# Kernel tuning notes

Hardware: AMD Instinct MI355X
Metric: run time of the kernel (lower is better)

## Reference

```python
import jax, jax.numpy as jnp
import numpy as np

B, L, K = 8, 1024, 30
NUM_RBF = 16
NPOS = 16
MAXREL = 32
EDGE = 128
EDGE_IN = NPOS + NUM_RBF * 25  # 416

# 25 atom-pair order (ProteinMPNN convention) over atoms [Ca=0, N=1, C=2, O=3, Cb=4]
PAIR_I = np.array([0,1,2,3,4,0,0,0,0,1,1,1,4,4,3,1,2,3,4,2,3,4,2,3,2])
PAIR_J = np.array([0,1,2,3,4,1,2,3,4,2,3,4,2,3,2,0,0,0,0,1,1,1,4,4,3])


def setup_inputs() -> dict:
    key = jax.random.key(0)
    ks = jax.random.split(key, 8)
    X = jax.random.normal(ks[0], (B, L, 4, 3), dtype=jnp.float32) * 3.0
    mask = jnp.ones((B, L), dtype=jnp.float32)
    residue_idx = jnp.arange(B * L, dtype=jnp.int64 if jax.config.jax_enable_x64 else jnp.int32).reshape(B, L)
    S = jax.random.randint(ks[1], (B, L), 0, 21)
    SSE3_seq = jax.random.randint(ks[2], (B, L), 0, 4)
    SSE8_seq = jax.random.randint(ks[3], (B, L), 0, 9)
    W_pos = jax.random.normal(ks[4], (2 * MAXREL + 2, NPOS), dtype=jnp.float32) * 0.02
    b_pos = jnp.zeros((NPOS,), dtype=jnp.float32)
    W_edge = jax.random.normal(ks[5], (EDGE_IN, EDGE), dtype=jnp.float32) * 0.02
    ln_gamma = jnp.ones((EDGE,), dtype=jnp.float32)
    ln_beta = jnp.zeros((EDGE,), dtype=jnp.float32)
    return {"X": X, "mask": mask, "residue_idx": residue_idx, "S": S,
            "SSE3_seq": SSE3_seq, "SSE8_seq": SSE8_seq,
            "W_pos": W_pos, "b_pos": b_pos, "W_edge": W_edge,
            "ln_gamma": ln_gamma, "ln_beta": ln_beta}


def _forward(X, mask, residue_idx, W_pos, b_pos, W_edge, ln_gamma, ln_beta):
    N = X[:, :, 0, :]
    Ca = X[:, :, 1, :]
    C = X[:, :, 2, :]
    O = X[:, :, 3, :]
    b = Ca - N
    c = C - Ca
    a = jnp.cross(b, c)
    Cb = -0.58273431 * a + 0.56802827 * b - 0.54067466 * c + Ca

    # _dist: masked pairwise Ca distances, k smallest
    mask2 = mask[:, :, None] * mask[:, None, :]                      # [B,L,L]
    D = mask2 * jnp.sqrt(jnp.sum((Ca[:, :, None] - Ca[:, None]) ** 2, -1) + 1e-6)
    D_max = jnp.max(D, axis=-1, keepdims=True)
    D_adjust = D + (1.0 - mask2) * D_max
    _, E_idx = jax.lax.top_k(-D_adjust, K)                           # [B,L,K] smallest

    # 25 atom-pair RBFs: gather neighbor atoms, then pairwise atom distances
    atoms = jnp.stack([Ca, N, C, O, Cb], axis=2)                     # [B,L,5,3]
    atoms_nb = jax.vmap(lambda a, i: a[i])(atoms, E_idx)             # [B,L,K,5,3]
    Dp = jnp.sqrt(jnp.sum((atoms[:, :, None, :, None, :] - atoms_nb[:, :, :, None, :, :]) ** 2, -1) + 1e-6)  # [B,L,K,5,5]
    mu = jnp.linspace(2.0, 22.0, NUM_RBF)
    sigma = (22.0 - 2.0) / NUM_RBF
    rbf = jnp.exp(-(((Dp[..., None] - mu) / sigma) ** 2))            # [B,L,K,5,5,R]
    rbf_all = rbf[:, :, :, PAIR_I, PAIR_J, :].reshape(Dp.shape[0], Dp.shape[1], K, 25 * NUM_RBF)

    # positional encodings of relative residue index
    offset = residue_idx[:, :, None] - residue_idx[:, None, :]       # [B,L,L]
    off_nb = jnp.take_along_axis(offset, E_idx, axis=2)              # [B,L,K]
    d = jnp.clip(off_nb + MAXREL, 0, 2 * MAXREL)
    E_pos = W_pos[d] + b_pos                                         # [B,L,K,NPOS]

    E = jnp.concatenate([E_pos, rbf_all], axis=-1) @ W_edge          # [B,L,K,EDGE]
    m = jnp.mean(E, axis=-1, keepdims=True)
    v = jnp.mean((E - m) ** 2, axis=-1, keepdims=True)
    E = (E - m) / jnp.sqrt(v + 1e-5) * ln_gamma + ln_beta
    return E, E_idx


def reference(X, mask, residue_idx, S, SSE3_seq, SSE8_seq, W_pos, b_pos, W_edge, ln_gamma, ln_beta):
    return _forward(X, mask, residue_idx, W_pos, b_pos, W_edge, ln_gamma, ln_beta)
```

## Files before the change

### kernel.cpp

```cpp
#include <hip/hip_runtime.h>

#define BB 8
#define LL 1024
#define KNB 30
#define NUM_RBF 16
#define NPOS 16
#define MAXREL 32
#define EDGE_C 128
#define EDGE_IN 416
#define NKK 26
#define WTF_N (NKK * 4 * 64 * 8)

__constant__ int PAIR_I_d[25] = {0,1,2,3,4,0,0,0,0,1,1,1,4,4,3,1,2,3,4,2,3,4,2,3,2};
__constant__ int PAIR_J_d[25] = {0,1,2,3,4,1,2,3,4,2,3,4,2,3,2,0,0,0,0,1,1,1,4,4,3};

typedef float floatx16 __attribute__((ext_vector_type(16)));

__global__ __launch_bounds__(256) void knn_kernel(const float* __restrict__ X,
                                                  const float* __restrict__ mask,
                                                  float* __restrict__ out_idx,
                                                  const float* __restrict__ W_edge,
                                                  unsigned char* __restrict__ WtF) {
    if (blockIdx.x >= 2048) {
        int o = (blockIdx.x - 2048) * 256 + threadIdx.x;
        if (o < WTF_N) {
            int j = o & 7, l = (o >> 3) & 63, w = (o >> 9) & 3, kk = o >> 11;
            int k = (kk << 4) + ((l >> 5) << 3) + j;
            int n = (w << 5) + (l & 31);
            float wv = W_edge[k * EDGE_C + n];
            int pk = __builtin_amdgcn_cvt_pk_fp8_f32(wv, wv, 0, false);
            WtF[o] = (unsigned char)(pk & 0xFF);
        }
        return;
    }

    int b = blockIdx.x >> 8;
    int i0 = (blockIdx.x & 255) * 4;
    int tid = threadIdx.x;
    int lane = tid & 63;
    int wv = tid >> 6;

    __shared__ float sCa[LL * 3];
    __shared__ float sMask[LL];

    for (int j = tid; j < LL; j += 256) {
        int base = (b * LL + j) * 12 + 3;
        sCa[j * 3 + 0] = X[base + 0];
        sCa[j * 3 + 1] = X[base + 1];
        sCa[j * 3 + 2] = X[base + 2];
        sMask[j] = mask[b * LL + j];
    }
    __syncthreads();

    int i = i0 + wv;
    int row = b * LL + i;
    float cax = sCa[i * 3 + 0], cay = sCa[i * 3 + 1], caz = sCa[i * 3 + 2];
    float mi = sMask[i];

    float Dv[16];
    float dmax = 0.0f;
#pragma unroll
    for (int c = 0; c < 16; ++c) {
        int j = lane + c * 64;
        float dx = cax - sCa[j * 3 + 0];
        float dy = cay - sCa[j * 3 + 1];
        float dz = caz - sCa[j * 3 + 2];
        float m2 = mi * sMask[j];
        float D = m2 * sqrtf(dx * dx + dy * dy + dz * dz + 1e-6f);
        Dv[c] = D;
        dmax = fmaxf(dmax, D);
    }
    for (int o = 32; o; o >>= 1) dmax = fmaxf(dmax, __shfl_down(dmax, o));
    dmax = __shfl(dmax, 0);

    double cand[16];
#pragma unroll
    for (int c = 0; c < 16; ++c) {
        int j = lane + c * 64;
        float m2 = mi * sMask[j];
        float Dadj = Dv[c] + (1.0f - m2) * dmax;
        unsigned int bits = __float_as_uint(Dadj);
        cand[c] = fma((double)bits, 1024.0, (double)j);
    }

    const double KILL = 9.0e15;
    float myj = 0.0f;
    for (int r = 0; r < KNB; ++r) {
        double a0 = fmin(cand[0], cand[1]);
        double a1 = fmin(cand[2], cand[3]);
        double a2 = fmin(cand[4], cand[5]);
        double a3 = fmin(cand[6], cand[7]);
        double a4 = fmin(cand[8], cand[9]);
        double a5 = fmin(cand[10], cand[11]);
        double a6 = fmin(cand[12], cand[13]);
        double a7 = fmin(cand[14], cand[15]);
        a0 = fmin(a0, a1); a2 = fmin(a2, a3); a4 = fmin(a4, a5); a6 = fmin(a6, a7);
        a0 = fmin(a0, a2); a4 = fmin(a4, a6);
        double m = fmin(a0, a4);
        for (int o = 32; o; o >>= 1) {
            double other = __shfl_down(m, o);
            m = fmin(m, other);
        }
        m = __shfl(m, 0);
        unsigned long long ku = (unsigned long long)m;
        int jw = __builtin_amdgcn_readfirstlane((int)(ku & 1023));
        bool own = (lane == (jw & 63));
        switch (jw >> 6) {
            case 0:  if (own) cand[0]  = KILL; break;
            case 1:  if (own) cand[1]  = KILL; break;
            case 2:  if (own) cand[2]  = KILL; break;
            case 3:  if (own) cand[3]  = KILL; break;
            case 4:  if (own) cand[4]  = KILL; break;
            case 5:  if (own) cand[5]  = KILL; break;
            case 6:  if (own) cand[6]  = KILL; break;
            case 7:  if (own) cand[7]  = KILL; break;
            case 8:  if (own) cand[8]  = KILL; break;
            case 9:  if (own) cand[9]  = KILL; break;
            case 10: if (own) cand[10] = KILL; break;
            case 11: if (own) cand[11] = KILL; break;
            case 12: if (own) cand[12] = KILL; break;
            case 13: if (own) cand[13] = KILL; break;
            case 14: if (own) cand[14] = KILL; break;
            case 15: if (own) cand[15] = KILL; break;
        }
        if (lane == r) myj = (float)jw;
    }
    if (lane < KNB) out_idx[(size_t)row * KNB + lane] = myj;
}

__global__ __launch_bounds__(256) void edge_kernel(const float* __restrict__ X,
                                                   const int* __restrict__ ridx,
                                                   const float* __restrict__ W_pos,
                                                   const float* __restrict__ b_pos,
                                                   const unsigned char* __restrict__ WtF,
                                                   const float* __restrict__ gamma,
                                                   const float* __restrict__ beta,
                                                   const float* __restrict__ out_idx,
                                                   float* __restrict__ out_E) {
    int row = blockIdx.x;
    int b = row >> 10;
    int i = row & 1023;
    int tid = threadIdx.x;

    __shared__ __align__(16) char smem[16384];
    unsigned char* fA = (unsigned char*)smem;
    float* Esh = (float*)smem;
    float* atoms = (float*)smem;
    float* dist = (float*)(smem + 13312);

    if (tid < 31) {
        int r = (tid == 0) ? i : (int)out_idx[(size_t)row * KNB + (tid - 1)];
        int base = (b * LL + r) * 12;
        float Nx = X[base + 0], Ny = X[base + 1], Nz = X[base + 2];
        float Cax = X[base + 3], Cay = X[base + 4], Caz = X[base + 5];
        float Cx = X[base + 6], Cy = X[base + 7], Cz = X[base + 8];
        float Ox = X[base + 9], Oy = X[base + 10], Oz = X[base + 11];
        float bx = Cax - Nx, by = Cay - Ny, bz = Caz - Nz;
        float cx = Cx - Cax, cy = Cy - Cay, cz = Cz - Caz;
        float ax = by * cz - bz * cy;
        float ay = bz * cx - bx * cz;
        float az = bx * cy - by * cx;
        float Cbx = -0.58273431f * ax + 0.56802827f * bx - 0.54067466f * cx + Cax;
        float Cby = -0.58273431f * ay + 0.56802827f * by - 0.54067466f * cy + Cay;
        float Cbz = -0.58273431f * az + 0.56802827f * bz - 0.54067466f * cz + Caz;
        float* A = &atoms[tid * 15];
        A[0] = Cax; A[1] = Cay; A[2] = Caz;
        A[3] = Nx;  A[4] = Ny;  A[5] = Nz;
        A[6] = Cx;  A[7] = Cy;  A[8] = Cz;
        A[9] = Ox;  A[10] = Oy; A[11] = Oz;
        A[12] = Cbx; A[13] = Cby; A[14] = Cbz;
    }
    __syncthreads();

    for (int idx = tid; idx < KNB * 25; idx += 256) {
        int k = idx / 25;
        int p = idx - k * 25;
        const float* Ai = &atoms[PAIR_I_d[p] * 3];
        const float* Aj = &atoms[(1 + k) * 15 + PAIR_J_d[p] * 3];
        float dx = Ai[0] - Aj[0], dy = Ai[1] - Aj[1], dz = Ai[2] - Aj[2];
        dist[idx] = __builtin_amdgcn_sqrtf(dx * dx + dy * dy + dz * dz + 1e-6f);
    }
    __syncthreads();

    {
        int m = tid & 31;
        int kgb = tid >> 5;
        float cbase = (kgb & 1) ? 14.4f : 5.8666668f;
        const float SQL2E = 1.2011224f;
        const float C1 = 3.0777494f;
        const float C0 = 1.6414664f;
        const float DK = 0.1027397f;
#pragma unroll
        for (int r = 0; r < 7; ++r) {
            int kg = kgb + 8 * r;
            if (kg < 52) {
                int lo, hi;
                if (m >= KNB) {
                    lo = 0; hi = 0;
                } else if (kg < 2) {
                    int jn = (int)out_idx[(size_t)row * KNB + m];
                    int off = ridx[row] - ridx[b * LL + jn] + MAXREL;
                    off = off < 0 ? 0 : (off > 2 * MAXREL ? 2 * MAXREL : off);
                    const float4* wp = (const float4*)&W_pos[off * NPOS + kg * 8];
                    const float4* bp = (const float4*)&b_pos[kg * 8];
                    float4 w0 = wp[0], w1 = wp[1];
                    float4 p0 = bp[0], p1 = bp[1];
                    lo = __builtin_amdgcn_cvt_pk_fp8_f32(w0.x + p0.x, w0.y + p0.y, 0, false);
                    lo = __builtin_amdgcn_cvt_pk_fp8_f32(w0.z + p0.z, w0.w + p0.w, lo, true);
                    hi = __builtin_amdgcn_cvt_pk_fp8_f32(w1.x + p1.x, w1.y + p1.y, 0, false);
                    hi = __builtin_amdgcn_cvt_pk_fp8_f32(w1.z + p1.z, w1.w + p1.w, hi, true);
                } else {
                    int p = (kg - 2) >> 1;
                    float d = dist[m * 25 + p];
                    float xc = fminf(fmaf(0.8f, d, -cbase), 12.0f);
                    float xs = xc * SQL2E;
                    float r4 = __builtin_amdgcn_exp2f(-xs * xs);
                    float fw = __builtin_amdgcn_exp2f(fmaf(C1, xc, -C0));
                    float bw = __builtin_amdgcn_exp2f(fmaf(-C1, xc, -C0));
                    float r5 = r4 * fw; fw *= DK;
                    float r6 = r5 * fw; fw *= DK;
                    float r7 = r6 * fw;
                    float r3 = r4 * bw; bw *= DK;
                    float r2 = r3 * bw; bw *= DK;
                    float r1 = r2 * bw; bw *= DK;
                    float r0 = r1 * bw;
                    lo = __builtin_amdgcn_cvt_pk_fp8_f32(r0, r1, 0, false);
                    lo = __builtin_amdgcn_cvt_pk_fp8_f32(r2, r3, lo, true);
                    hi = __builtin_amdgcn_cvt_pk_fp8_f32(r4, r5, 0, false);
                    hi = __builtin_amdgcn_cvt_pk_fp8_f32(r6, r7, hi, true);
                }
                int pos = ((kg >> 1) * 64 + m + 32 * (kg & 1)) * 8;
                long v = ((long)(unsigned int)hi << 32) | (unsigned int)lo;
                *(long*)(fA + pos) = v;
            }
        }
    }
    __syncthreads();

    int wv = tid >> 6;
    int l = tid & 63;
    floatx16 acc;
#pragma unroll
    for (int r = 0; r < 16; ++r) acc[r] = 0.0f;

    const long* Ap = (const long*)fA + l;
    const long* Bp = (const long*)WtF + wv * 64 + l;
#pragma unroll 4
    for (int kk = 0; kk < NKK; ++kk) {
        long a = Ap[kk * 64];
        long bfr = Bp[kk * 256];
        acc = __builtin_amdgcn_mfma_f32_32x32x16_fp8_fp8(a, bfr, acc, 0, 0, 0);
    }
    __syncthreads();

#pragma unroll
    for (int r = 0; r < 16; ++r) {
        int rr = (r & 3) + 8 * (r >> 2) + 4 * (l >> 5);
        Esh[rr * EDGE_C + wv * 32 + (l & 31)] = acc[r];
    }
    __syncthreads();

    int cg = tid & 31;
    int ky = tid >> 5;
    int c0 = cg * 4;
    float gam0 = gamma[c0 + 0], gam1 = gamma[c0 + 1];
    float gam2 = gamma[c0 + 2], gam3 = gamma[c0 + 3];
    float bet0 = beta[c0 + 0], bet1 = beta[c0 + 1];
    float bet2 = beta[c0 + 2], bet3 = beta[c0 + 3];

#pragma unroll
    for (int r2 = 0; r2 < 4; ++r2) {
        int e = ky + 8 * r2;
        float4 v = *(const float4*)&Esh[e * EDGE_C + c0];
        float s = (v.x + v.y) + (v.z + v.w);
        float q = fmaf(v.x, v.x, fmaf(v.y, v.y, fmaf(v.z, v.z, v.w * v.w)));
#pragma unroll
        for (int o = 16; o; o >>= 1) {
            s += __shfl_xor(s, o);
            q += __shfl_xor(q, o);
        }
        float mean = s * 0.0078125f;
        float var = fmaf(-mean, mean, q * 0.0078125f);
        float inv = __builtin_amdgcn_rsqf(var + 1e-5f);
        if (e < KNB) {
            float ig0 = inv * gam0, ig1 = inv * gam1;
            float ig2 = inv * gam2, ig3 = inv * gam3;
            float4 o4;
            o4.x = fmaf(v.x, ig0, fmaf(-mean, ig0, bet0));
            o4.y = fmaf(v.y, ig1, fmaf(-mean, ig1, bet1));
            o4.z = fmaf(v.z, ig2, fmaf(-mean, ig2, bet2));
            o4.w = fmaf(v.w, ig3, fmaf(-mean, ig3, bet3));
            *(float4*)(out_E + ((size_t)(row * KNB + e)) * EDGE_C + c0) = o4;
        }
    }
}

extern "C" void kernel_launch(void* const* d_in, const int* in_sizes, int n_in,
                              void* d_out, int out_size, void* d_ws, size_t ws_size,
                              hipStream_t stream) {
    const float* X      = (const float*)d_in[0];
    const float* mask   = (const float*)d_in[1];
    const int*   ridx   = (const int*)d_in[2];
    const float* W_pos  = (const float*)d_in[6];
    const float* b_pos  = (const float*)d_in[7];
    const float* W_edge = (const float*)d_in[8];
    const float* gamma  = (const float*)d_in[9];
    const float* beta   = (const float*)d_in[10];

    float* out_E   = (float*)d_out;
    float* out_idx = out_E + (size_t)BB * LL * KNB * EDGE_C;
    unsigned char* WtF = (unsigned char*)d_ws;

    int knn_grid = 2048 + (WTF_N + 255) / 256;
    knn_kernel<<<knn_grid, 256, 0, stream>>>(X, mask, out_idx, W_edge, WtF);
    edge_kernel<<<BB * LL, 256, 0, stream>>>(X, ridx, W_pos, b_pos, WtF,
                                             gamma, beta, out_idx, out_E);
}
```

Measured before the change: 238.5 us.

## Fuse kNN selection and edge feature kernels into one per-4-row kernel

Merges the kNN top-k kernel and the edge RBF/MFMA/layernorm kernel into a single kernel in which each 256-thread block finds neighbors for 4 residues and then processes those 4 rows sequentially. Neighbor indices are passed through shared memory instead of a global round trip, and the weight fp8 prep moves into a separate small kernel. This removes one large launch and the reload of neighbor indices, but cuts the edge-stage grid to a quarter of its previous block count, with four serialized passes per block and more barriers, so occupancy and latency hiding may drop.

Result: slower. 267.7 us (+12.2%).

```diff
diff --git a/kernel.cpp b/kernel.cpp
--- a/kernel.cpp
+++ b/kernel.cpp
@@ -16,32 +16,44 @@
 
 typedef float floatx16 __attribute__((ext_vector_type(16)));
 
-__global__ __launch_bounds__(256) void knn_kernel(const float* __restrict__ X,
-                                                  const float* __restrict__ mask,
-                                                  float* __restrict__ out_idx,
-                                                  const float* __restrict__ W_edge,
-                                                  unsigned char* __restrict__ WtF) {
-    if (blockIdx.x >= 2048) {
-        int o = (blockIdx.x - 2048) * 256 + threadIdx.x;
-        if (o < WTF_N) {
-            int j = o & 7, l = (o >> 3) & 63, w = (o >> 9) & 3, kk = o >> 11;
-            int k = (kk << 4) + ((l >> 5) << 3) + j;
-            int n = (w << 5) + (l & 31);
-            float wv = W_edge[k * EDGE_C + n];
-            int pk = __builtin_amdgcn_cvt_pk_fp8_f32(wv, wv, 0, false);
-            WtF[o] = (unsigned char)(pk & 0xFF);
-        }
-        return;
+__global__ __launch_bounds__(256) void wprep_kernel(const float* __restrict__ W_edge,
+                                                    unsigned char* __restrict__ WtF) {
+    int o = blockIdx.x * 256 + threadIdx.x;
+    if (o < WTF_N) {
+        int j = o & 7, l = (o >> 3) & 63, w = (o >> 9) & 3, kk = o >> 11;
+        int k = (kk << 4) + ((l >> 5) << 3) + j;
+        int n = (w << 5) + (l & 31);
+        float wv = W_edge[k * EDGE_C + n];
+        int pk = __builtin_amdgcn_cvt_pk_fp8_f32(wv, wv, 0, false);
+        WtF[o] = (unsigned char)(pk & 0xFF);
     }
-
+}
+
+__global__ __launch_bounds__(256) void fused_kernel(const float* __restrict__ X,
+                                                    const float* __restrict__ mask,
+                                                    const int* __restrict__ ridx,
+                                                    const float* __restrict__ W_pos,
+                                                    const float* __restrict__ b_pos,
+                                                    const unsigned char* __restrict__ WtF,
+                                                    const float* __restrict__ gamma,
+                                                    const float* __restrict__ beta,
+                                                    float* __restrict__ out_idx,
+                                                    float* __restrict__ out_E) {
     int b = blockIdx.x >> 8;
     int i0 = (blockIdx.x & 255) * 4;
     int tid = threadIdx.x;
     int lane = tid & 63;
     int wv = tid >> 6;
-
-    __shared__ float sCa[LL * 3];
-    __shared__ float sMask[LL];
+    int l = lane;
+
+    __shared__ __align__(16) char smem[16896];
+    float* sCa  = (float*)smem;
+    float* sMask = (float*)(smem + 12288);
+    int*   nbrL = (int*)(smem + 16384);
+    unsigned char* fA = (unsigned char*)smem;
+    float* Esh = (float*)smem;
+    float* atoms = (float*)smem;
+    float* dist = (float*)(smem + 13312);
 
     for (int j = tid; j < LL; j += 256) {
         int base = (b * LL + j) * 12 + 3;
@@ -52,214 +64,88 @@
     }
     __syncthreads();
 
-    int i = i0 + wv;
-    int row = b * LL + i;
-    float cax = sCa[i * 3 + 0], cay = sCa[i * 3 + 1], caz = sCa[i * 3 + 2];
-    float mi = sMask[i];
-
-    float Dv[16];
-    float dmax = 0.0f;
-#pragma unroll
-    for (int c = 0; c < 16; ++c) {
-        int j = lane + c * 64;
-        float dx = cax - sCa[j * 3 + 0];
-        float dy = cay - sCa[j * 3 + 1];
-        float dz = caz - sCa[j * 3 + 2];
-        float m2 = mi * sMask[j];
-        float D = m2 * sqrtf(dx * dx + dy * dy + dz * dz + 1e-6f);
-        Dv[c] = D;
-        dmax = fmaxf(dmax, D);
-    }
-    for (int o = 32; o; o >>= 1) dmax = fmaxf(dmax, __shfl_down(dmax, o));
-    dmax = __shfl(dmax, 0);
-
-    double cand[16];
-#pragma unroll
-    for (int c = 0; c < 16; ++c) {
-        int j = lane + c * 64;
-        float m2 = mi * sMask[j];
-        float Dadj = Dv[c] + (1.0f - m2) * dmax;
-        unsigned int bits = __float_as_uint(Dadj);
-        cand[c] = fma((double)bits, 1024.0, (double)j);
-    }
-
-    const double KILL = 9.0e15;
-    float myj = 0.0f;
-    for (int r = 0; r < KNB; ++r) {
-        double a0 = fmin(cand[0], cand[1]);
-        double a1 = fmin(cand[2], cand[3]);
-        double a2 = fmin(cand[4], cand[5]);
-        double a3 = fmin(cand[6], cand[7]);
-        double a4 = fmin(cand[8], cand[9]);
-        double a5 = fmin(cand[10], cand[11]);
-        double a6 = fmin(cand[12], cand[13]);
-        double a7 = fmin(cand[14], cand[15]);
-        a0 = fmin(a0, a1); a2 = fmin(a2, a3); a4 = fmin(a4, a5); a6 = fmin(a6, a7);
-        a0 = fmin(a0, a2); a4 = fmin(a4, a6);
-        double m = fmin(a0, a4);
-        for (int o = 32; o; o >>= 1) {
-            double other = __shfl_down(m, o);
-            m = fmin(m, other);
-        }
-        m = __shfl(m, 0);
-        unsigned long long ku = (unsigned long long)m;
-        int jw = __builtin_amdgcn_readfirstlane((int)(ku & 1023));
-        bool own = (lane == (jw & 63));
-        switch (jw >> 6) {
-            case 0:  if (own) cand[0]  = KILL; break;
-            case 1:  if (own) cand[1]  = KILL; break;
-            case 2:  if (own) cand[2]  = KILL; break;
-            case 3:  if (own) cand[3]  = KILL; break;
-            case 4:  if (own) cand[4]  = KILL; break;
-            case 5:  if (own) cand[5]  = KILL; break;
-            case 6:  if (own) cand[6]  = KILL; break;
-            case 7:  if (own) cand[7]  = KILL; break;
-            case 8:  if (own) cand[8]  = KILL; break;
-            case 9:  if (own) cand[9]  = KILL; break;
-            case 10: if (own) cand[10] = KILL; break;
-            case 11: if (own) cand[11] = KILL; break;
-            case 12: if (own) cand[12] = KILL; break;
-            case 13: if (own) cand[13] = KILL; break;
-            case 14: if (own) cand[14] = KILL; break;
-            case 15: if (own) cand[15] = KILL; break;
-        }
-        if (lane == r) myj = (float)jw;
-    }
-    if (lane < KNB) out_idx[(size_t)row * KNB + lane] = myj;
-}
-
-__global__ __launch_bounds__(256) void edge_kernel(const float* __restrict__ X,
-                                                   const int* __restrict__ ridx,
-                                                   const float* __restrict__ W_pos,
-                                                   const float* __restrict__ b_pos,
-                                                   const unsigned char* __restrict__ WtF,
-                                                   const float* __restrict__ gamma,
-                                                   const float* __restrict__ beta,
-                                                   const float* __restrict__ out_idx,
-                                                   float* __restrict__ out_E) {
-    int row = blockIdx.x;
-    int b = row >> 10;
-    int i = row & 1023;
-    int tid = threadIdx.x;
-
-    __shared__ __align__(16) char smem[16384];
-    unsigned char* fA = (unsigned char*)smem;
-    float* Esh = (float*)smem;
-    float* atoms = (float*)smem;
-    float* dist = (float*)(smem + 13312);
-
-    if (tid < 31) {
-        int r = (tid == 0) ? i : (int)out_idx[(size_t)row * KNB + (tid - 1)];
-        int base = (b * LL + r) * 12;
-        float Nx = X[base + 0], Ny = X[base + 1], Nz = X[base + 2];
-        float Cax = X[base + 3], Cay = X[base + 4], Caz = X[base + 5];
-        float Cx = X[base + 6], Cy = X[base + 7], Cz = X[base + 8];
-        float Ox = X[base + 9], Oy = X[base + 10], Oz = X[base + 11];
-        float bx = Cax - Nx, by = Cay - Ny, bz = Caz - Nz;
-        float cx = Cx - Cax, cy = Cy - Cay, cz = Cz - Caz;
-        float ax = by * cz - bz * cy;
-        float ay = bz * cx - bx * cz;
-        float az = bx * cy - by * cx;
-        float Cbx = -0.58273431f * ax + 0.56802827f * bx - 0.54067466f * cx + Cax;
-        float Cby = -0.58273431f * ay + 0.56802827f * by - 0.54067466f * cy + Cay;
-        float Cbz = -0.58273431f * az + 0.56802827f * bz - 0.54067466f * cz + Caz;
-        float* A = &atoms[tid * 15];
-        A[0] = Cax; A[1] = Cay; A[2] = Caz;
-        A[3] = Nx;  A[4] = Ny;  A[5] = Nz;
-        A[6] = Cx;  A[7] = Cy;  A[8] = Cz;
-        A[9] = Ox;  A[10] = Oy; A[11] = Oz;
-        A[12] = Cbx; A[13] = Cby; A[14] = Cbz;
+    {
+        int i = i0 + wv;
+        int row = b * LL + i;
+        float cax = sCa[i * 3 + 0], cay = sCa[i * 3 + 1], caz = sCa[i * 3 + 2];
+        float mi = sMask[i];
+
+        float Dv[16];
+        float dmax = 0.0f;
+#pragma unroll
+        for (int c = 0; c < 16; ++c) {
+            int j = lane + c * 64;
+            float dx = cax - sCa[j * 3 + 0];
+            float dy = cay - sCa[j * 3 + 1];
+            float dz = caz - sCa[j * 3 + 2];
+            float m2 = mi * sMask[j];
+            float D = m2 * sqrtf(dx * dx + dy * dy + dz * dz + 1e-6f);
+            Dv[c] = D;
+            dmax = fmaxf(dmax, D);
+        }
+        for (int o = 32; o; o >>= 1) dmax = fmaxf(dmax, __shfl_down(dmax, o));
+        dmax = __shfl(dmax, 0);
+
+        double cand[16];
+#pragma unroll
+        for (int c = 0; c < 16; ++c) {
+            int j = lane + c * 64;
+            float m2 = mi * sMask[j];
+            float Dadj = Dv[c] + (1.0f - m2) * dmax;
+            unsigned int bits = __float_as_uint(Dadj);
+            cand[c] = fma((double)bits, 1024.0, (double)j);
+        }
+
+        const double KILL = 9.0e15;
+        float myj = 0.0f;
+        for (int r = 0; r < KNB; ++r) {
+            double a0 = fmin(cand[0], cand[1]);
+            double a1 = fmin(cand[2], cand[3]);
+            double a2 = fmin(cand[4], cand[5]);
+            double a3 = fmin(cand[6], cand[7]);
+            double a4 = fmin(cand[8], cand[9]);
+            double a5 = fmin(cand[10], cand[11]);
+            double a6 = fmin(cand[12], cand[13]);
+            double a7 = fmin(cand[14], cand[15]);
+            a0 = fmin(a0, a1); a2 = fmin(a2, a3); a4 = fmin(a4, a5); a6 = fmin(a6, a7);
+            a0 = fmin(a0, a2); a4 = fmin(a4, a6);
+            double m = fmin(a0, a4);
+            for (int o = 32; o; o >>= 1) {
+                double other = __shfl_down(m, o);
+                m = fmin(m, other);
+            }
+            m = __shfl(m, 0);
+            unsigned long long ku = (unsigned long long)m;
+            int jw = __builtin_amdgcn_readfirstlane((int)(ku & 1023));
+            bool own = (lane == (jw & 63));
+            switch (jw >> 6) {
+                case 0:  if (own) cand[0]  = KILL; break;
+                case 1:  if (own) cand[1]  = KILL; break;
+                case 2:  if (own) cand[2]  = KILL; break;
+                case 3:  if (own) cand[3]  = KILL; break;
+                case 4:  if (own) cand[4]  = KILL; break;
+                case 5:  if (own) cand[5]  = KILL; break;
+                case 6:  if (own) cand[6]  = KILL; break;
+                case 7:  if (own) cand[7]  = KILL; break;
+                case 8:  if (own) cand[8]  = KILL; break;
+                case 9:  if (own) cand[9]  = KILL; break;
+                case 10: if (own) cand[10] = KILL; break;
+                case 11: if (own) cand[11] = KILL; break;
+                case 12: if (own) cand[12] = KILL; break;
+                case 13: if (own) cand[13] = KILL; break;
+                case 14: if (own) cand[14] = KILL; break;
+                case 15: if (own) cand[15] = KILL; break;
+            }
+            if (lane == r) myj = (float)jw;
+        }
+        if (lane < KNB) {
+            out_idx[(size_t)row * KNB + lane] = myj;
+            nbrL[wv * KNB + lane] = (int)myj;
+        }
     }
     __syncthreads();
 
-    for (int idx = tid; idx < KNB * 25; idx += 256) {
-        int k = idx / 25;
-        int p = idx - k * 25;
-        const float* Ai = &atoms[PAIR_I_d[p] * 3];
-        const float* Aj = &atoms[(1 + k) * 15 + PAIR_J_d[p] * 3];
-        float dx = Ai[0] - Aj[0], dy = Ai[1] - Aj[1], dz = Ai[2] - Aj[2];
-        dist[idx] = __builtin_amdgcn_sqrtf(dx * dx + dy * dy + dz * dz + 1e-6f);
-    }
-    __syncthreads();
-
-    {
-        int m = tid & 31;
-        int kgb = tid >> 5;
-        float cbase = (kgb & 1) ? 14.4f : 5.8666668f;
-        const float SQL2E = 1.2011224f;
-        const float C1 = 3.0777494f;
-        const float C0 = 1.6414664f;
-        const float DK = 0.1027397f;
-#pragma unroll
-        for (int r = 0; r < 7; ++r) {
-            int kg = kgb + 8 * r;
-            if (kg < 52) {
-                int lo, hi;
-                if (m >= KNB) {
-                    lo = 0; hi = 0;
-                } else if (kg < 2) {
-                    int jn = (int)out_idx[(size_t)row * KNB + m];
-                    int off = ridx[row] - ridx[b * LL + jn] + MAXREL;
-                    off = off < 0 ? 0 : (off > 2 * MAXREL ? 2 * MAXREL : off);
-                    const float4* wp = (const float4*)&W_pos[off * NPOS + kg * 8];
-                    const float4* bp = (const float4*)&b_pos[kg * 8];
-                    float4 w0 = wp[0], w1 = wp[1];
-                    float4 p0 = bp[0], p1 = bp[1];
-                    lo = __builtin_amdgcn_cvt_pk_fp8_f32(w0.x + p0.x, w0.y + p0.y, 0, false);
-                    lo = __builtin_amdgcn_cvt_pk_fp8_f32(w0.z + p0.z, w0.w + p0.w, lo, true);
-                    hi = __builtin_amdgcn_cvt_pk_fp8_f32(w1.x + p1.x, w1.y + p1.y, 0, false);
-                    hi = __builtin_amdgcn_cvt_pk_fp8_f32(w1.z + p1.z, w1.w + p1.w, hi, true);
-                } else {
-                    int p = (kg - 2) >> 1;
-                    float d = dist[m * 25 + p];
-                    float xc = fminf(fmaf(0.8f, d, -cbase), 12.0f);
-                    float xs = xc * SQL2E;
-                    float r4 = __builtin_amdgcn_exp2f(-xs * xs);
-                    float fw = __builtin_amdgcn_exp2f(fmaf(C1, xc, -C0));
-                    float bw = __builtin_amdgcn_exp2f(fmaf(-C1, xc, -C0));
-                    float r5 = r4 * fw; fw *= DK;
-                    float r6 = r5 * fw; fw *= DK;
-                    float r7 = r6 * fw;
-                    float r3 = r4 * bw; bw *= DK;
-                    float r2 = r3 * bw; bw *= DK;
-                    float r1 = r2 * bw; bw *= DK;
-                    float r0 = r1 * bw;
-                    lo = __builtin_amdgcn_cvt_pk_fp8_f32(r0, r1, 0, false);
-                    lo = __builtin_amdgcn_cvt_pk_fp8_f32(r2, r3, lo, true);
-                    hi = __builtin_amdgcn_cvt_pk_fp8_f32(r4, r5, 0, false);
-                    hi = __builtin_amdgcn_cvt_pk_fp8_f32(r6, r7, hi, true);
-                }
-                int pos = ((kg >> 1) * 64 + m + 32 * (kg & 1)) * 8;
-                long v = ((long)(unsigned int)hi << 32) | (unsigned int)lo;
-                *(long*)(fA + pos) = v;
-            }
-        }
-    }
-    __syncthreads();
-
-    int wv = tid >> 6;
-    int l = tid & 63;
-    floatx16 acc;
-#pragma unroll
-    for (int r = 0; r < 16; ++r) acc[r] = 0.0f;
-
-    const long* Ap = (const long*)fA + l;
     const long* Bp = (const long*)WtF + wv * 64 + l;
-#pragma unroll 4
-    for (int kk = 0; kk < NKK; ++kk) {
-        long a = Ap[kk * 64];
-        long bfr = Bp[kk * 256];
-        acc = __builtin_amdgcn_mfma_f32_32x32x16_fp8_fp8(a, bfr, acc, 0, 0, 0);
-    }
-    __syncthreads();
-
-#pragma unroll
-    for (int r = 0; r < 16; ++r) {
-        int rr = (r & 3) + 8 * (r >> 2) + 4 * (l >> 5);
-        Esh[rr * EDGE_C + wv * 32 + (l & 31)] = acc[r];
-    }
-    __syncthreads();
-
     int cg = tid & 31;
     int ky = tid >> 5;
     int c0 = cg * 4;
@@ -268,30 +154,144 @@
     float bet0 = beta[c0 + 0], bet1 = beta[c0 + 1];
     float bet2 = beta[c0 + 2], bet3 = beta[c0 + 3];
 
-#pragma unroll
-    for (int r2 = 0; r2 < 4; ++r2) {
-        int e = ky + 8 * r2;
-        float4 v = *(const float4*)&Esh[e * EDGE_C + c0];
-        float s = (v.x + v.y) + (v.z + v.w);
-        float q = fmaf(v.x, v.x, fmaf(v.y, v.y, fmaf(v.z, v.z, v.w * v.w)));
-#pragma unroll
-        for (int o = 16; o; o >>= 1) {
-            s += __shfl_xor(s, o);
-            q += __shfl_xor(q, o);
-        }
-        float mean = s * 0.0078125f;
-        float var = fmaf(-mean, mean, q * 0.0078125f);
-        float inv = __builtin_amdgcn_rsqf(var + 1e-5f);
-        if (e < KNB) {
-            float ig0 = inv * gam0, ig1 = inv * gam1;
-            float ig2 = inv * gam2, ig3 = inv * gam3;
-            float4 o4;
-            o4.x = fmaf(v.x, ig0, fmaf(-mean, ig0, bet0));
-            o4.y = fmaf(v.y, ig1, fmaf(-mean, ig1, bet1));
-            o4.z = fmaf(v.z, ig2, fmaf(-mean, ig2, bet2));
-            o4.w = fmaf(v.w, ig3, fmaf(-mean, ig3, bet3));
-            *(float4*)(out_E + ((size_t)(row * KNB + e)) * EDGE_C + c0) = o4;
-        }
+    for (int q = 0; q < 4; ++q) {
+        int i = i0 + q;
+        int row = b * LL + i;
+
+        if (tid < 31) {
+            int r = (tid == 0) ? i : nbrL[q * KNB + (tid - 1)];
+            int base = (b * LL + r) * 12;
+            float Nx = X[base + 0], Ny = X[base + 1], Nz = X[base + 2];
+            float Cax = X[base + 3], Cay = X[base + 4], Caz = X[base + 5];
+            float Cx = X[base + 6], Cy = X[base + 7], Cz = X[base + 8];
+            float Ox = X[base + 9], Oy = X[base + 10], Oz = X[base + 11];
+            float bx = Cax - Nx, by = Cay - Ny, bz = Caz - Nz;
+            float cx = Cx - Cax, cy = Cy - Cay, cz = Cz - Caz;
+            float ax = by * cz - bz * cy;
+            float ay = bz * cx - bx * cz;
+            float az = bx * cy - by * cx;
+            float Cbx = -0.58273431f * ax + 0.56802827f * bx - 0.54067466f * cx + Cax;
+            float Cby = -0.58273431f * ay + 0.56802827f * by - 0.54067466f * cy + Cay;
+            float Cbz = -0.58273431f * az + 0.56802827f * bz - 0.54067466f * cz + Caz;
+            float* A = &atoms[tid * 15];
+            A[0] = Cax; A[1] = Cay; A[2] = Caz;
+            A[3] = Nx;  A[4] = Ny;  A[5] = Nz;
+            A[6] = Cx;  A[7] = Cy;  A[8] = Cz;
+            A[9] = Ox;  A[10] = Oy; A[11] = Oz;
+            A[12] = Cbx; A[13] = Cby; A[14] = Cbz;
+        }
+        __syncthreads();
+
+        for (int idx = tid; idx < KNB * 25; idx += 256) {
+            int k = idx / 25;
+            int p = idx - k * 25;
+            const float* Ai = &atoms[PAIR_I_d[p] * 3];
+            const float* Aj = &atoms[(1 + k) * 15 + PAIR_J_d[p] * 3];
+            float dx = Ai[0] - Aj[0], dy = Ai[1] - Aj[1], dz = Ai[2] - Aj[2];
+            dist[idx] = __builtin_amdgcn_sqrtf(dx * dx + dy * dy + dz * dz + 1e-6f);
+        }
+        __syncthreads();
+
+        {
+            int m = tid & 31;
+            int kgb = tid >> 5;
+            float cbase = (kgb & 1) ? 14.4f : 5.8666668f;
+            const float SQL2E = 1.2011224f;
+            const float C1 = 3.0777494f;
+            const float C0 = 1.6414664f;
+            const float DK = 0.1027397f;
+#pragma unroll
+            for (int r = 0; r < 7; ++r) {
+                int kg = kgb + 8 * r;
+                if (kg < 52) {
+                    int lo, hi;
+                    if (m >= KNB) {
+                        lo = 0; hi = 0;
+                    } else if (kg < 2) {
+                        int jn = nbrL[q * KNB + m];
+                        int off = ridx[row] - ridx[b * LL + jn] + MAXREL;
+                        off = off < 0 ? 0 : (off > 2 * MAXREL ? 2 * MAXREL : off);
+                        const float4* wp = (const float4*)&W_pos[off * NPOS + kg * 8];
+                        const float4* bp = (const float4*)&b_pos[kg * 8];
+                        float4 w0 = wp[0], w1 = wp[1];
+                        float4 p0 = bp[0], p1 = bp[1];
+                        lo = __builtin_amdgcn_cvt_pk_fp8_f32(w0.x + p0.x, w0.y + p0.y, 0, false);
+                        lo = __builtin_amdgcn_cvt_pk_fp8_f32(w0.z + p0.z, w0.w + p0.w, lo, true);
+                        hi = __builtin_amdgcn_cvt_pk_fp8_f32(w1.x + p1.x, w1.y + p1.y, 0, false);
+                        hi = __builtin_amdgcn_cvt_pk_fp8_f32(w1.z + p1.z, w1.w + p1.w, hi, true);
+                    } else {
+                        int p = (kg - 2) >> 1;
+                        float d = dist[m * 25 + p];
+                        float xc = fminf(fmaf(0.8f, d, -cbase), 12.0f);
+                        float xs = xc * SQL2E;
+                        float r4 = __builtin_amdgcn_exp2f(-xs * xs);
+                        float fw = __builtin_amdgcn_exp2f(fmaf(C1, xc, -C0));
+                        float bw = __builtin_amdgcn_exp2f(fmaf(-C1, xc, -C0));
+                        float r5 = r4 * fw; fw *= DK;
+                        float r6 = r5 * fw; fw *= DK;
+                        float r7 = r6 * fw;
+                        float r3 = r4 * bw; bw *= DK;
+                        float r2 = r3 * bw; bw *= DK;
+                        float r1 = r2 * bw; bw *= DK;
+                        float r0 = r1 * bw;
+                        lo = __builtin_amdgcn_cvt_pk_fp8_f32(r0, r1, 0, false);
+                        lo = __builtin_amdgcn_cvt_pk_fp8_f32(r2, r3, lo, true);
+                        hi = __builtin_amdgcn_cvt_pk_fp8_f32(r4, r5, 0, false);
+                        hi = __builtin_amdgcn_cvt_pk_fp8_f32(r6, r7, hi, true);
+                    }
+                    int pos = ((kg >> 1) * 64 + m + 32 * (kg & 1)) * 8;
+                    long v = ((long)(unsigned int)hi << 32) | (unsigned int)lo;
+                    *(long*)(fA + pos) = v;
+                }
+            }
+        }
+        __syncthreads();
+
+        floatx16 acc;
+#pragma unroll
+        for (int r = 0; r < 16; ++r) acc[r] = 0.0f;
+        const long* Ap = (const long*)fA + l;
+#pragma unroll 4
+        for (int kk = 0; kk < NKK; ++kk) {
+            long a = Ap[kk * 64];
+            long bfr = Bp[kk * 256];
+            acc = __builtin_amdgcn_mfma_f32_32x32x16_fp8_fp8(a, bfr, acc, 0, 0, 0);
+        }
+        __syncthreads();
+
+#pragma unroll
+        for (int r = 0; r < 16; ++r) {
+            int rr = (r & 3) + 8 * (r >> 2) + 4 * (l >> 5);
+            Esh[rr * EDGE_C + wv * 32 + (l & 31)] = acc[r];
+        }
+        __syncthreads();
+
+#pragma unroll
+        for (int r2 = 0; r2 < 4; ++r2) {
+            int e = ky + 8 * r2;
+            float4 v = *(const float4*)&Esh[e * EDGE_C + c0];
+            float s = (v.x + v.y) + (v.z + v.w);
+            float qq = fmaf(v.x, v.x, fmaf(v.y, v.y, fmaf(v.z, v.z, v.w * v.w)));
+#pragma unroll
+            for (int o = 16; o; o >>= 1) {
+                s += __shfl_xor(s, o);
+                qq += __shfl_xor(qq, o);
+            }
+            float mean = s * 0.0078125f;
+            float var = fmaf(-mean, mean, qq * 0.0078125f);
+            float inv = __builtin_amdgcn_rsqf(var + 1e-5f);
+            if (e < KNB) {
+                float ig0 = inv * gam0, ig1 = inv * gam1;
+                float ig2 = inv * gam2, ig3 = inv * gam3;
+                float4 o4;
+                o4.x = fmaf(v.x, ig0, fmaf(-mean, ig0, bet0));
+                o4.y = fmaf(v.y, ig1, fmaf(-mean, ig1, bet1));
+                o4.z = fmaf(v.z, ig2, fmaf(-mean, ig2, bet2));
+                o4.w = fmaf(v.w, ig3, fmaf(-mean, ig3, bet3));
+                *(float4*)(out_E + ((size_t)(row * KNB + e)) * EDGE_C + c0) = o4;
+            }
+        }
+        __syncthreads();
     }
 }
 
@@ -311,8 +311,7 @@
     float* out_idx = out_E + (size_t)BB * LL * KNB * EDGE_C;
     unsigned char* WtF = (unsigned char*)d_ws;
 
-    int knn_grid = 2048 + (WTF_N + 255) / 256;
-    knn_kernel<<<knn_grid, 256, 0, stream>>>(X, mask, out_idx, W_edge, WtF);
-    edge_kernel<<<BB * LL, 256, 0, stream>>>(X, ridx, W_pos, b_pos, WtF,
-                                             gamma, beta, out_idx, out_E);
+    wprep_kernel<<<(WTF_N + 255) / 256, 256, 0, stream>>>(W_edge, WtF);
+    fused_kernel<<<BB * LL / 4, 256, 0, stream>>>(X, mask, ridx, W_pos, b_pos, WtF,
+                                                  gamma, beta, out_idx, out_E);
 }
```

## Process two residue rows per edge-kernel block with 512 threads

Applied to the files above, without the earlier changes.

The edge kernel now handles two query residues per block, using 512 threads and 8 waves laid out as a 2x4 tile over rows and output columns. Shared memory grows to 32KB to hold both rows' atoms, distances, fp8 A tiles and the E staging buffer. The aim is to halve the block count and amortise per-block setup and the W fragment loads across two rows. The cost is larger blocks with more LDS each, which may reduce occupancy.

Measured after the change: 242.4 us. About the same (+1.7%).

```diff
diff --git a/kernel.cpp b/kernel.cpp
--- a/kernel.cpp
+++ b/kernel.cpp
@@ -128,7 +128,7 @@
     if (lane < KNB) out_idx[(size_t)row * KNB + lane] = myj;
 }
 
-__global__ __launch_bounds__(256) void edge_kernel(const float* __restrict__ X,
+__global__ __launch_bounds__(512) void edge_kernel(const float* __restrict__ X,
                                                    const int* __restrict__ ridx,
                                                    const float* __restrict__ W_pos,
                                                    const float* __restrict__ b_pos,
@@ -137,19 +137,22 @@
                                                    const float* __restrict__ beta,
                                                    const float* __restrict__ out_idx,
                                                    float* __restrict__ out_E) {
-    int row = blockIdx.x;
-    int b = row >> 10;
-    int i = row & 1023;
+    int b = blockIdx.x >> 9;
+    int i0 = (blockIdx.x & 511) * 2;
     int tid = threadIdx.x;
-
-    __shared__ __align__(16) char smem[16384];
-    unsigned char* fA = (unsigned char*)smem;
+    int lane = tid & 63;
+
+    __shared__ __align__(16) char smem[32768];
+    float* dist  = (float*)smem;
+    float* atoms = (float*)(smem + 6016);
+    unsigned char* fA = (unsigned char*)(smem + 6144);
     float* Esh = (float*)smem;
-    float* atoms = (float*)smem;
-    float* dist = (float*)(smem + 13312);
-
-    if (tid < 31) {
-        int r = (tid == 0) ? i : (int)out_idx[(size_t)row * KNB + (tid - 1)];
+
+    if (tid < 62) {
+        int q = tid >= 31 ? 1 : 0;
+        int tt = tid - 31 * q;
+        int rowq = b * LL + i0 + q;
+        int r = (tt == 0) ? (i0 + q) : (int)out_idx[(size_t)rowq * KNB + (tt - 1)];
         int base = (b * LL + r) * 12;
         float Nx = X[base + 0], Ny = X[base + 1], Nz = X[base + 2];
         float Cax = X[base + 3], Cay = X[base + 4], Caz = X[base + 5];
@@ -163,7 +166,7 @@
         float Cbx = -0.58273431f * ax + 0.56802827f * bx - 0.54067466f * cx + Cax;
         float Cby = -0.58273431f * ay + 0.56802827f * by - 0.54067466f * cy + Cay;
         float Cbz = -0.58273431f * az + 0.56802827f * bz - 0.54067466f * cz + Caz;
-        float* A = &atoms[tid * 15];
+        float* A = &atoms[(q * 31 + tt) * 15];
         A[0] = Cax; A[1] = Cay; A[2] = Caz;
         A[3] = Nx;  A[4] = Ny;  A[5] = Nz;
         A[6] = Cx;  A[7] = Cy;  A[8] = Cz;
@@ -172,34 +175,39 @@
     }
     __syncthreads();
 
-    for (int idx = tid; idx < KNB * 25; idx += 256) {
-        int k = idx / 25;
-        int p = idx - k * 25;
-        const float* Ai = &atoms[PAIR_I_d[p] * 3];
-        const float* Aj = &atoms[(1 + k) * 15 + PAIR_J_d[p] * 3];
+    for (int idx = tid; idx < 2 * KNB * 25; idx += 512) {
+        int t = idx >= 750 ? 1 : 0;
+        int rem = idx - 750 * t;
+        int k = rem / 25;
+        int p = rem - k * 25;
+        const float* Ai = &atoms[(t * 31) * 15 + PAIR_I_d[p] * 3];
+        const float* Aj = &atoms[(t * 31 + 1 + k) * 15 + PAIR_J_d[p] * 3];
         float dx = Ai[0] - Aj[0], dy = Ai[1] - Aj[1], dz = Ai[2] - Aj[2];
         dist[idx] = __builtin_amdgcn_sqrtf(dx * dx + dy * dy + dz * dz + 1e-6f);
     }
     __syncthreads();
 
     {
-        int m = tid & 31;
-        int kgb = tid >> 5;
+        int m = tid & 63;
+        int t = m >> 5;
+        int mm = m & 31;
+        int kgb = tid >> 6;
         float cbase = (kgb & 1) ? 14.4f : 5.8666668f;
         const float SQL2E = 1.2011224f;
         const float C1 = 3.0777494f;
         const float C0 = 1.6414664f;
         const float DK = 0.1027397f;
+        int rowq = b * LL + i0 + t;
 #pragma unroll
         for (int r = 0; r < 7; ++r) {
             int kg = kgb + 8 * r;
             if (kg < 52) {
                 int lo, hi;
-                if (m >= KNB) {
+                if (mm >= KNB) {
                     lo = 0; hi = 0;
                 } else if (kg < 2) {
-                    int jn = (int)out_idx[(size_t)row * KNB + m];
-                    int off = ridx[row] - ridx[b * LL + jn] + MAXREL;
+                    int jn = (int)out_idx[(size_t)rowq * KNB + mm];
+                    int off = ridx[rowq] - ridx[b * LL + jn] + MAXREL;
                     off = off < 0 ? 0 : (off > 2 * MAXREL ? 2 * MAXREL : off);
                     const float4* wp = (const float4*)&W_pos[off * NPOS + kg * 8];
                     const float4* bp = (const float4*)&b_pos[kg * 8];
@@ -211,7 +219,7 @@
                     hi = __builtin_amdgcn_cvt_pk_fp8_f32(w1.z + p1.z, w1.w + p1.w, hi, true);
                 } else {
                     int p = (kg - 2) >> 1;
-                    float d = dist[m * 25 + p];
+                    float d = dist[t * 750 + mm * 25 + p];
                     float xc = fminf(fmaf(0.8f, d, -cbase), 12.0f);
                     float xs = xc * SQL2E;
                     float r4 = __builtin_amdgcn_exp2f(-xs * xs);
@@ -229,7 +237,7 @@
                     hi = __builtin_amdgcn_cvt_pk_fp8_f32(r4, r5, 0, false);
                     hi = __builtin_amdgcn_cvt_pk_fp8_f32(r6, r7, hi, true);
                 }
-                int pos = ((kg >> 1) * 64 + m + 32 * (kg & 1)) * 8;
+                int pos = t * 13312 + ((kg >> 1) * 64 + mm + 32 * (kg & 1)) * 8;
                 long v = ((long)(unsigned int)hi << 32) | (unsigned int)lo;
                 *(long*)(fA + pos) = v;
             }
@@ -238,13 +246,14 @@
     __syncthreads();
 
     int wv = tid >> 6;
-    int l = tid & 63;
+    int wr = wv >> 2;
+    int wc = wv & 3;
     floatx16 acc;
 #pragma unroll
     for (int r = 0; r < 16; ++r) acc[r] = 0.0f;
 
-    const long* Ap = (const long*)fA + l;
-    const long* Bp = (const long*)WtF + wv * 64 + l;
+    const long* Ap = (const long*)(fA + wr * 13312) + lane;
+    const long* Bp = (const long*)WtF + wc * 64 + lane;
 #pragma unroll 4
     for (int kk = 0; kk < NKK; ++kk) {
         long a = Ap[kk * 64];
@@ -255,8 +264,8 @@
 
 #pragma unroll
     for (int r = 0; r < 16; ++r) {
-        int rr = (r & 3) + 8 * (r >> 2) + 4 * (l >> 5);
-        Esh[rr * EDGE_C + wv * 32 + (l & 31)] = acc[r];
+        int rr = (r & 3) + 8 * (r >> 2) + 4 * (lane >> 5);
+        Esh[(wr * 32 + rr) * EDGE_C + wc * 32 + (lane & 31)] = acc[r];
     }
     __syncthreads();
 
@@ -270,19 +279,21 @@
 
 #pragma unroll
     for (int r2 = 0; r2 < 4; ++r2) {
-        int e = ky + 8 * r2;
+        int e = ky + 16 * r2;
+        int t = e >> 5;
+        int el = e & 31;
         float4 v = *(const float4*)&Esh[e * EDGE_C + c0];
         float s = (v.x + v.y) + (v.z + v.w);
-        float q = fmaf(v.x, v.x, fmaf(v.y, v.y, fmaf(v.z, v.z, v.w * v.w)));
+        float qq = fmaf(v.x, v.x, fmaf(v.y, v.y, fmaf(v.z, v.z, v.w * v.w)));
 #pragma unroll
         for (int o = 16; o; o >>= 1) {
             s += __shfl_xor(s, o);
-            q += __shfl_xor(q, o);
+            qq += __shfl_xor(qq, o);
         }
         float mean = s * 0.0078125f;
-        float var = fmaf(-mean, mean, q * 0.0078125f);
+        float var = fmaf(-mean, mean, qq * 0.0078125f);
         float inv = __builtin_amdgcn_rsqf(var + 1e-5f);
-        if (e < KNB) {
+        if (el < KNB) {
             float ig0 = inv * gam0, ig1 = inv * gam1;
             float ig2 = inv * gam2, ig3 = inv * gam3;
             float4 o4;
@@ -290,7 +301,8 @@
             o4.y = fmaf(v.y, ig1, fmaf(-mean, ig1, bet1));
             o4.z = fmaf(v.z, ig2, fmaf(-mean, ig2, bet2));
             o4.w = fmaf(v.w, ig3, fmaf(-mean, ig3, bet3));
-            *(float4*)(out_E + ((size_t)(row * KNB + e)) * EDGE_C + c0) = o4;
+            size_t orow = (size_t)(b * LL + i0 + t) * KNB + el;
+            *(float4*)(out_E + orow * EDGE_C + c0) = o4;
         }
     }
 }
@@ -313,6 +325,6 @@
 
     int knn_grid = 2048 + (WTF_N + 255) / 256;
     knn_kernel<<<knn_grid, 256, 0, stream>>>(X, mask, out_idx, W_edge, WtF);
-    edge_kernel<<<BB * LL, 256, 0, stream>>>(X, ridx, W_pos, b_pos, WtF,
-                                             gamma, beta, out_idx, out_E);
+    edge_kernel<<<BB * LL / 2, 512, 0, stream>>>(X, ridx, W_pos, b_pos, WtF,
+                                                 gamma, beta, out_idx, out_E);
 }
```
